# Performance work log

Measured on AMD Instinct MI355X. Metric: run time of the kernel, lower is better.

Reference implementation:

```python
import jax, jax.numpy as jnp
import numpy as np
from jax import lax

B, N1, F1 = 8, 8192, 64
N2, K = 1024, 32
RADIUS = 0.2
MLP_SIZES = [64, 64, 128]
IN_DIM = 3 + F1  # concat(local xyz, features)


def _glorot_uniform(key, fan_in, fan_out):
    lim = np.sqrt(6.0 / (fan_in + fan_out)).astype(np.float32)
    return jax.random.uniform(key, (fan_in, fan_out), jnp.float32, -lim, lim)


def setup_inputs() -> dict:
    key = jax.random.key(0)
    ks = jax.random.split(key, 2 + len(MLP_SIZES))
    xyz = jax.random.uniform(ks[0], (B, N1, 3), jnp.float32)
    features = jax.random.normal(ks[1], (B, N1, F1), jnp.float32)
    inp = {"xyz": xyz, "features": features}
    d = IN_DIM
    for i, m in enumerate(MLP_SIZES):
        inp[f"W{i}"] = _glorot_uniform(ks[2 + i], d, m)
        inp[f"b{i}"] = jnp.zeros((m,), jnp.float32)
        d = m
    return inp


def farthest_point_sample(xyz, n_sample):
    # xyz: (B, N, 3) -> (B, n_sample) int32 indices. Sequential greedy FPS via scan.
    Bb, N, _ = xyz.shape
    first = jnp.zeros((Bb,), jnp.int32)
    big = jnp.finfo(xyz.dtype).max

    def step(carry, _):
        min_d, last = carry
        p = jnp.take_along_axis(xyz, last[:, None, None], axis=1)  # (B,1,3)
        d = jnp.sum((xyz - p) ** 2, axis=-1)                        # (B,N)
        min_d = jnp.minimum(min_d, d)
        nxt = jnp.argmax(min_d, axis=1).astype(jnp.int32)
        return (min_d, nxt), nxt

    init = (jnp.full((Bb, N), big, xyz.dtype), first)
    _, rest = lax.scan(step, init, None, length=n_sample - 1)  # (n_sample-1, B)
    return jnp.concatenate([first[None, :], rest], axis=0).T    # (B, n_sample)


def knn_search(query, points, k, radius):
    # query: (B,N2,3), points: (B,N1,3) -> (B,N2,k) indices, radius-clamped
    q2 = jnp.sum(query ** 2, -1)[:, :, None]          # (B,N2,1)
    p2 = jnp.sum(points ** 2, -1)[:, None, :]         # (B,1,N1)
    qp = jnp.einsum('bqd,bnd->bqn', query, points)    # (B,N2,N1)
    d2 = q2 + p2 - 2.0 * qp
    neg, idx = lax.top_k(-d2, k)                       # k nearest
    d2k = -neg
    # neighbors beyond the radius are replaced by the closest neighbor (ball query)
    idx = jnp.where(d2k > radius * radius, idx[..., :1], idx)
    return idx, d2k


def _gather_pts(x, idx):
    # x: (B,N1,C), idx: (B,N2[,K]) -> batched gather along axis 1
    return jnp.take_along_axis(x, idx.reshape(x.shape[0], -1, 1), axis=1).reshape(
        idx.shape + (x.shape[-1],))


def reference(xyz, features, W0, b0, W1, b1, W2, b2):
    sel_idx = farthest_point_sample(xyz, N2)                    # (B,N2)
    selected_xyz = _gather_pts(xyz, sel_idx)                    # (B,N2,3)
    nbr_idx, _ = knn_search(selected_xyz, xyz, K, RADIUS)       # (B,N2,K)
    nbr_xyz = _gather_pts(xyz, nbr_idx) - selected_xyz[:, :, None, :]
    nbr_feat = _gather_pts(features, nbr_idx)                   # (B,N2,K,F1)
    h = jnp.concatenate([nbr_xyz, nbr_feat], axis=-1)           # (B,N2,K,3+F1)
    for W, b in ((W0, b0), (W1, b1), (W2, b2)):
        h = jax.nn.leaky_relu(jnp.einsum('bqkc,cm->bqkm', h, W) + b, 0.2)
    selected_features = jnp.max(h, axis=2)                      # (B,N2,F2)
    return selected_xyz, selected_features
```

## Files before the change

kernel.cpp:

```cpp
#include <hip/hip_runtime.h>

#define B_   8
#define N1_  8192
#define N2_  1024
#define K_   32
#define F1_  64
#define CIN_ 67
#define M1_  64
#define M2_  64
#define M3_  128
#define HSTR 40
#define FLTMAX 3.402823466e+38f

#define FNW  4
#define PPT  32

__device__ __forceinline__ unsigned f2key(float f) {
  unsigned u = __float_as_uint(f);
  return u ^ ((unsigned)((int)u >> 31) | 0x80000000u);
}

__device__ __forceinline__ unsigned dpp_umax_bcast(unsigned v) {
  unsigned o;
  o = (unsigned)__builtin_amdgcn_update_dpp(0, (int)v, 0x111, 0xf, 0xf, false); v = v > o ? v : o;
  o = (unsigned)__builtin_amdgcn_update_dpp(0, (int)v, 0x112, 0xf, 0xf, false); v = v > o ? v : o;
  o = (unsigned)__builtin_amdgcn_update_dpp(0, (int)v, 0x114, 0xf, 0xf, false); v = v > o ? v : o;
  o = (unsigned)__builtin_amdgcn_update_dpp(0, (int)v, 0x118, 0xf, 0xf, false); v = v > o ? v : o;
  o = (unsigned)__builtin_amdgcn_update_dpp(0, (int)v, 0x142, 0xf, 0xf, false); v = v > o ? v : o;
  o = (unsigned)__builtin_amdgcn_update_dpp(0, (int)v, 0x143, 0xf, 0xf, false); v = v > o ? v : o;
  return (unsigned)__builtin_amdgcn_readlane((int)v, 63);
}
__device__ __forceinline__ unsigned dpp_umin_bcast(unsigned v) {
  unsigned o;
  o = (unsigned)__builtin_amdgcn_update_dpp(-1, (int)v, 0x111, 0xf, 0xf, false); v = v < o ? v : o;
  o = (unsigned)__builtin_amdgcn_update_dpp(-1, (int)v, 0x112, 0xf, 0xf, false); v = v < o ? v : o;
  o = (unsigned)__builtin_amdgcn_update_dpp(-1, (int)v, 0x114, 0xf, 0xf, false); v = v < o ? v : o;
  o = (unsigned)__builtin_amdgcn_update_dpp(-1, (int)v, 0x118, 0xf, 0xf, false); v = v < o ? v : o;
  o = (unsigned)__builtin_amdgcn_update_dpp(-1, (int)v, 0x142, 0xf, 0xf, false); v = v < o ? v : o;
  o = (unsigned)__builtin_amdgcn_update_dpp(-1, (int)v, 0x143, 0xf, 0xf, false); v = v < o ? v : o;
  return (unsigned)__builtin_amdgcn_readlane((int)v, 63);
}

#define HS_ENC(f) (__float_as_uint(f) ^ 0xC0000000u)
#define HS_DEC(u) __uint_as_float((u) ^ 0xC0000000u)

__global__ __launch_bounds__(256, 1) void fused_kernel(
    const float* __restrict__ xyz, const float* __restrict__ feat,
    const float* __restrict__ w0g, const float* __restrict__ b0g,
    const float* __restrict__ w1g, const float* __restrict__ b1g,
    const float* __restrict__ w2g, const float* __restrict__ b2g,
    float* __restrict__ out_xyz, float* __restrict__ out_feat)
{
  __shared__ float4 wslot[2][FNW];
  __shared__ __align__(16) float buf0[CIN_*HSTR];
  __shared__ __align__(16) float buf1[M1_*HSTR];
  __shared__ float sval[2][4];
  __shared__ int   sidx[2][4];
  __shared__ float qsh[3];

  const int t = threadIdx.x;
  const int lane = t & 63;

  if (blockIdx.x < B_) {
    __builtin_amdgcn_s_setprio(3);
    const int b = blockIdx.x;
    const float* gxyz = xyz + (size_t)b * (N1_ * 3);
    float* oxyz = out_xyz + (size_t)b * (N2_ * 3);

    float x[PPT], y[PPT], z[PPT], md[PPT];
    {
      const float4* gs = (const float4*)gxyz;
#pragma unroll
      for (int w = 0; w < 24; ++w) {
        const float4 v = gs[t * 24 + w];
#pragma unroll
        for (int c = 0; c < 4; ++c) {
          const int p = w * 4 + c;
          const float val = (c == 0) ? v.x : (c == 1) ? v.y : (c == 2) ? v.z : v.w;
          const int j = p / 3, cc = p % 3;
          if (cc == 0) x[j] = val; else if (cc == 1) y[j] = val; else z[j] = val;
        }
      }
    }
#pragma unroll
    for (int j = 0; j < PPT; ++j) md[j] = FLTMAX;

    const int wv_ = t >> 6;
    if (lane == 0) { float4 s; s.x = -1.0f; s.y = 0.f; s.z = 0.f; s.w = 0.f; wslot[1][wv_] = s; }
    if (t == 0)   { float4 s; s.x = 1.0f; s.y = x[0]; s.z = y[0]; s.w = z[0]; wslot[1][0] = s; }
    __syncthreads();

    for (int i = 1; i < N2_; ++i) {
      const int p = i & 1;
      float4 wb = wslot[p][0];
#pragma unroll
      for (int u = 1; u < FNW; ++u) { const float4 s = wslot[p][u]; if (s.x > wb.x) wb = s; }
      const float px = wb.y, py = wb.z, pz = wb.w;
      if (t == 0) {
        const int g = (b << 10) + (i - 1);
        const int o = (i - 1) * 3;
        oxyz[o] = px; oxyz[o+1] = py; oxyz[o+2] = pz;
        unsigned* hs = (unsigned*)(out_feat + (size_t)g * M3_);
        atomicExch(&hs[0], HS_ENC(px));
        atomicExch(&hs[1], HS_ENC(py));
        atomicExch(&hs[2], HS_ENC(pz));
      }

      float bestv, bx, by, bz;
#pragma unroll
      for (int j = 0; j < PPT; ++j) {
        const float dx = __fsub_rn(x[j], px);
        const float dy = __fsub_rn(y[j], py);
        const float dz = __fsub_rn(z[j], pz);
        const float d  = __fadd_rn(__fadd_rn(__fmul_rn(dx,dx), __fmul_rn(dy,dy)), __fmul_rn(dz,dz));
        md[j] = fminf(md[j], d);
        if (j == 0) { bestv = md[0]; bx = x[0]; by = y[0]; bz = z[0]; }
        else {
          const bool c = md[j] > bestv;
          bestv = c ? md[j] : bestv;
          bx = c ? x[j] : bx; by = c ? y[j] : by; bz = c ? z[j] : bz;
        }
      }
      const unsigned key = f2key(bestv);
      const unsigned kmax = dpp_umax_bcast(key);
      const int fl = __ffsll(__ballot(key == kmax)) - 1;
      if (lane == fl) {
        float4 s; s.x = bestv; s.y = bx; s.z = by; s.w = bz;
        wslot[1 - p][wv_] = s;
      }
      __syncthreads();
    }
    if (t == 0) {
      float4 wb = wslot[0][0];
#pragma unroll
      for (int u = 1; u < FNW; ++u) { const float4 s = wslot[0][u]; if (s.x > wb.x) wb = s; }
      const int g = (b << 10) + (N2_ - 1);
      const int o = (N2_ - 1) * 3;
      oxyz[o] = wb.y; oxyz[o+1] = wb.z; oxyz[o+2] = wb.w;
      unsigned* hs = (unsigned*)(out_feat + (size_t)g * M3_);
      atomicExch(&hs[0], HS_ENC(wb.y));
      atomicExch(&hs[1], HS_ENC(wb.z));
      atomicExch(&hs[2], HS_ENC(wb.w));
    }
    return;
  }

  const int bq = blockIdx.x - B_;
  const int b  = bq >> 10;
  const float* gxyz = xyz + (size_t)b * (N1_ * 3);

  if (t == 0) {
    unsigned* hs = (unsigned*)(out_feat + (size_t)bq * M3_);
#pragma unroll
    for (int w = 0; w < 3; ++w) {
      unsigned v;
      do { __builtin_amdgcn_s_sleep(2); v = atomicOr(&hs[w], 0u); }
      while (v == 0u || v == 0xAAAAAAAAu);
      qsh[w] = HS_DEC(v);
    }
  }
  __syncthreads();
  const float qx = qsh[0], qy = qsh[1], qz = qsh[2];
  const float q2 = __fadd_rn(__fadd_rn(__fmul_rn(qx,qx), __fmul_rn(qy,qy)), __fmul_rn(qz,qz));

  float d2v[32];
  float m1 = FLTMAX, m2 = FLTMAX; int i1 = t*32, i2 = t*32;
  {
    const float4* gs = (const float4*)gxyz;
#pragma unroll
    for (int g8 = 0; g8 < 4; ++g8) {
      float f[24];
#pragma unroll
      for (int w = 0; w < 6; ++w) {
        const float4 v = gs[t * 24 + g8 * 6 + w];
        f[w*4+0] = v.x; f[w*4+1] = v.y; f[w*4+2] = v.z; f[w*4+3] = v.w;
      }
#pragma unroll
      for (int m = 0; m < 8; ++m) {
        const int j = g8 * 8 + m;
        const float px = f[3*m], py = f[3*m+1], pz = f[3*m+2];
        const float p2 = __fadd_rn(__fadd_rn(__fmul_rn(px,px), __fmul_rn(py,py)), __fmul_rn(pz,pz));
        const float qp = __fadd_rn(__fadd_rn(__fmul_rn(qx,px), __fmul_rn(qy,py)), __fmul_rn(qz,pz));
        const float d  = __fsub_rn(__fadd_rn(q2, p2), __fmul_rn(2.0f, qp));
        d2v[j] = d;
        const int idx = t*32 + j;
        const bool c1 = d < m1;
        const bool c2 = d < m2;
        const float nm2 = c1 ? m1 : (c2 ? d : m2);
        const int   ni2 = c1 ? i1 : (c2 ? idx : i2);
        m1 = c1 ? d : m1; i1 = c1 ? idx : i1;
        m2 = nm2; i2 = ni2;
      }
    }
  }

  int myk_idx = 0; float myk_d = 0.0f; int k0_idx = 0;
  unsigned removed = 0u; bool have2 = true;
  for (int kk = 0; kk < K_; ++kk) {
    const int p = kk & 1;
    const unsigned key = f2key(m1);
    const unsigned kmin = dpp_umin_bcast(key);
    const int fl = __ffsll(__ballot(key == kmin)) - 1;
    if (lane == fl) { sval[p][t >> 6] = m1; sidx[p][t >> 6] = i1; }
    __syncthreads();
    float wv = sval[p][0]; int wi = sidx[p][0];
#pragma unroll
    for (int u = 1; u < 4; ++u) {
      const float v = sval[p][u]; const int ii = sidx[p][u];
      if (v < wv || (v == wv && ii < wi)) { wv = v; wi = ii; }
    }
    wi &= (N1_ - 1);
    if ((t >> 3) == kk) { myk_idx = wi; myk_d = wv; }
    if (kk == 0) k0_idx = wi;
    if (kk < K_ - 1 && t == (wi >> 5)) {
      removed |= 1u << (wi & 31);
      if (have2) { m1 = m2; i1 = i2; have2 = false; }
      else {
        m1 = FLTMAX; i1 = t*32; m2 = FLTMAX; i2 = t*32;
#pragma unroll
        for (int j = 0; j < 32; ++j) {
          const float d = ((removed >> j) & 1u) ? FLTMAX : d2v[j];
          const int idx = t*32 + j;
          const bool c1 = d < m1;
          const bool c2 = d < m2;
          const float nm2 = c1 ? m1 : (c2 ? d : m2);
          const int   ni2 = c1 ? i1 : (c2 ? idx : i2);
          m1 = c1 ? d : m1; i1 = c1 ? idx : i1;
          m2 = nm2; i2 = ni2;
        }
        have2 = true;
      }
    }
  }

  {
    const int k = t >> 3, fg = t & 7;
    int nk = myk_idx;
    if (myk_d > 0.04f) nk = k0_idx;
    nk &= (N1_ - 1);
    const float* frow = feat + ((size_t)(b * N1_ + nk)) * F1_ + fg * 8;
    const float4 f0 = *(const float4*)frow;
    const float4 f1 = *(const float4*)(frow + 4);
    const int fb = 3 + fg * 8;
    buf0[(fb+0)*HSTR + k] = f0.x;
    buf0[(fb+1)*HSTR + k] = f0.y;
    buf0[(fb+2)*HSTR + k] = f0.z;
    buf0[(fb+3)*HSTR + k] = f0.w;
    buf0[(fb+4)*HSTR + k] = f1.x;
    buf0[(fb+5)*HSTR + k] = f1.y;
    buf0[(fb+6)*HSTR + k] = f1.z;
    buf0[(fb+7)*HSTR + k] = f1.w;
    if (fg < 3) {
      const float pc = gxyz[(size_t)nk * 3 + fg];
      const float qc = (fg == 0) ? qx : (fg == 1) ? qy : qz;
      buf0[fg * HSTR + k] = __fsub_rn(pc, qc);
    }
  }
  __syncthreads();

#define LEAKY_STORE2(acc, mi_, biasg, hout) { \
    const float bb = biasg[mg*2 + (mi_)]; \
    float4 v; \
    v.x = acc.x + bb; v.x = fmaxf(v.x, 0.2f*v.x); \
    v.y = acc.y + bb; v.y = fmaxf(v.y, 0.2f*v.y); \
    v.z = acc.z + bb; v.z = fmaxf(v.z, 0.2f*v.z); \
    v.w = acc.w + bb; v.w = fmaxf(v.w, 0.2f*v.w); \
    *(float4*)&hout[(mg*2 + (mi_)) * HSTR + kq * 4] = v; }

  {
    const int kq = t & 7, mg = t >> 3;
    float4 a0 = {0,0,0,0}, a1 = {0,0,0,0};
#pragma unroll 4
    for (int c = 0; c < CIN_; ++c) {
      const float2 wp = *(const float2*)&w0g[c * M1_ + mg * 2];
      const float4 h  = *(const float4*)&buf0[c * HSTR + kq * 4];
      a0.x += h.x*wp.x; a0.y += h.y*wp.x; a0.z += h.z*wp.x; a0.w += h.w*wp.x;
      a1.x += h.x*wp.y; a1.y += h.y*wp.y; a1.z += h.z*wp.y; a1.w += h.w*wp.y;
    }
    LEAKY_STORE2(a0, 0, b0g, buf1) LEAKY_STORE2(a1, 1, b0g, buf1)
  }
  __syncthreads();

  {
    const int kq = t & 7, mg = t >> 3;
    float4 a0 = {0,0,0,0}, a1 = {0,0,0,0};
#pragma unroll 4
    for (int c = 0; c < M1_; ++c) {
      const float2 wp = *(const float2*)&w1g[c * M2_ + mg * 2];
      const float4 h  = *(const float4*)&buf1[c * HSTR + kq * 4];
      a0.x += h.x*wp.x; a0.y += h.y*wp.x; a0.z += h.z*wp.x; a0.w += h.w*wp.x;
      a1.x += h.x*wp.y; a1.y += h.y*wp.y; a1.z += h.z*wp.y; a1.w += h.w*wp.y;
    }
    LEAKY_STORE2(a0, 0, b1g, buf0) LEAKY_STORE2(a1, 1, b1g, buf0)
  }
#undef LEAKY_STORE2
  __syncthreads();

  {
    const int kq = t & 7, mg = t >> 3;
    float4 a0 = {0,0,0,0}, a1 = {0,0,0,0}, a2 = {0,0,0,0}, a3 = {0,0,0,0};
#pragma unroll 4
    for (int c = 0; c < M2_; ++c) {
      const float4 wp = *(const float4*)&w2g[c * M3_ + mg * 4];
      const float4 h  = *(const float4*)&buf0[c * HSTR + kq * 4];
      a0.x += h.x*wp.x; a0.y += h.y*wp.x; a0.z += h.z*wp.x; a0.w += h.w*wp.x;
      a1.x += h.x*wp.y; a1.y += h.y*wp.y; a1.z += h.z*wp.y; a1.w += h.w*wp.y;
      a2.x += h.x*wp.z; a2.y += h.y*wp.z; a2.z += h.z*wp.z; a2.w += h.w*wp.z;
      a3.x += h.x*wp.w; a3.y += h.y*wp.w; a3.z += h.z*wp.w; a3.w += h.w*wp.w;
    }
    float vm[4];
#define BIAS_LEAKY_HMAX(acc, mi_) { \
      const float bb = b2g[mg*4 + (mi_)]; \
      float vx = acc.x + bb; vx = fmaxf(vx, 0.2f*vx); \
      float vy = acc.y + bb; vy = fmaxf(vy, 0.2f*vy); \
      float vz = acc.z + bb; vz = fmaxf(vz, 0.2f*vz); \
      float vw = acc.w + bb; vw = fmaxf(vw, 0.2f*vw); \
      vm[mi_] = fmaxf(fmaxf(vx, vy), fmaxf(vz, vw)); }
    BIAS_LEAKY_HMAX(a0, 0) BIAS_LEAKY_HMAX(a1, 1) BIAS_LEAKY_HMAX(a2, 2) BIAS_LEAKY_HMAX(a3, 3)
#undef BIAS_LEAKY_HMAX
#pragma unroll
    for (int m = 1; m <= 4; m <<= 1) {
      vm[0] = fmaxf(vm[0], __shfl_xor(vm[0], m, 64));
      vm[1] = fmaxf(vm[1], __shfl_xor(vm[1], m, 64));
      vm[2] = fmaxf(vm[2], __shfl_xor(vm[2], m, 64));
      vm[3] = fmaxf(vm[3], __shfl_xor(vm[3], m, 64));
    }
    if (kq == 0) {
      float4 o; o.x = vm[0]; o.y = vm[1]; o.z = vm[2]; o.w = vm[3];
      *(float4*)&out_feat[(size_t)bq * M3_ + mg * 4] = o;
    }
  }
}

extern "C" void kernel_launch(void* const* d_in, const int* in_sizes, int n_in,
                              void* d_out, int out_size, void* d_ws, size_t ws_size,
                              hipStream_t stream) {
  const float* xyz  = (const float*)d_in[0];
  const float* feat = (const float*)d_in[1];
  const float* w0   = (const float*)d_in[2];
  const float* b0   = (const float*)d_in[3];
  const float* w1   = (const float*)d_in[4];
  const float* b1   = (const float*)d_in[5];
  const float* w2   = (const float*)d_in[6];
  const float* b2   = (const float*)d_in[7];

  float* out_xyz  = (float*)d_out;
  float* out_feat = out_xyz + B_ * N2_ * 3;

  fused_kernel<<<B_ + B_ * N2_, 256, 0, stream>>>(xyz, feat, w0, b0, w1, b1, w2, b2,
                                                  out_xyz, out_feat);
}
```

Measured before the change: 1.474 ms.

## Double threads per block to 512 and re-split FPS, kNN and MLP work

Raises the block size from 256 to 512 threads. Each thread now handles 16 points instead of 32 in FPS and kNN, and the kNN selection, feature gather and the three MLP layers are re-partitioned so each thread computes half as many output channels. The intent is to cut the per-thread serial latency of the sequential FPS loop and of the per-query top-k passes. In exchange, every reduction step spans twice as many waves and barriers, and the FPS blocks, which spin-wait against the query blocks, may see occupancy change.

```diff
diff --git a/kernel.cpp b/kernel.cpp
--- a/kernel.cpp
+++ b/kernel.cpp
@@ -12,8 +12,10 @@
 #define HSTR 40
 #define FLTMAX 3.402823466e+38f
 
-#define FNW  4
-#define PPT  32
+#define TPB  512
+#define FNW  (TPB/64)
+#define PPT  (N1_/TPB)
+#define PPC  16
 
 __device__ __forceinline__ unsigned f2key(float f) {
   unsigned u = __float_as_uint(f);
@@ -44,7 +46,7 @@
 #define HS_ENC(f) (__float_as_uint(f) ^ 0xC0000000u)
 #define HS_DEC(u) __uint_as_float((u) ^ 0xC0000000u)
 
-__global__ __launch_bounds__(256, 1) void fused_kernel(
+__global__ __launch_bounds__(TPB, 1) void fused_kernel(
     const float* __restrict__ xyz, const float* __restrict__ feat,
     const float* __restrict__ w0g, const float* __restrict__ b0g,
     const float* __restrict__ w1g, const float* __restrict__ b1g,
@@ -54,12 +56,13 @@
   __shared__ float4 wslot[2][FNW];
   __shared__ __align__(16) float buf0[CIN_*HSTR];
   __shared__ __align__(16) float buf1[M1_*HSTR];
-  __shared__ float sval[2][4];
-  __shared__ int   sidx[2][4];
+  __shared__ float sval[2][FNW];
+  __shared__ int   sidx[2][FNW];
   __shared__ float qsh[3];
 
   const int t = threadIdx.x;
   const int lane = t & 63;
+  const int wv_ = t >> 6;
 
   if (blockIdx.x < B_) {
     __builtin_amdgcn_s_setprio(3);
@@ -71,8 +74,8 @@
     {
       const float4* gs = (const float4*)gxyz;
 #pragma unroll
-      for (int w = 0; w < 24; ++w) {
-        const float4 v = gs[t * 24 + w];
+      for (int w = 0; w < 12; ++w) {
+        const float4 v = gs[t * 12 + w];
 #pragma unroll
         for (int c = 0; c < 4; ++c) {
           const int p = w * 4 + c;
@@ -85,7 +88,6 @@
 #pragma unroll
     for (int j = 0; j < PPT; ++j) md[j] = FLTMAX;
 
-    const int wv_ = t >> 6;
     if (lane == 0) { float4 s; s.x = -1.0f; s.y = 0.f; s.z = 0.f; s.w = 0.f; wslot[1][wv_] = s; }
     if (t == 0)   { float4 s; s.x = 1.0f; s.y = x[0]; s.z = y[0]; s.w = z[0]; wslot[1][0] = s; }
     __syncthreads();
@@ -163,16 +165,16 @@
   const float qx = qsh[0], qy = qsh[1], qz = qsh[2];
   const float q2 = __fadd_rn(__fadd_rn(__fmul_rn(qx,qx), __fmul_rn(qy,qy)), __fmul_rn(qz,qz));
 
-  float d2v[32];
-  float m1 = FLTMAX, m2 = FLTMAX; int i1 = t*32, i2 = t*32;
+  float d2v[PPC];
+  float m1 = FLTMAX, m2 = FLTMAX; int i1 = t*PPC, i2 = t*PPC;
   {
     const float4* gs = (const float4*)gxyz;
 #pragma unroll
-    for (int g8 = 0; g8 < 4; ++g8) {
+    for (int g8 = 0; g8 < 2; ++g8) {
       float f[24];
 #pragma unroll
       for (int w = 0; w < 6; ++w) {
-        const float4 v = gs[t * 24 + g8 * 6 + w];
+        const float4 v = gs[t * 12 + g8 * 6 + w];
         f[w*4+0] = v.x; f[w*4+1] = v.y; f[w*4+2] = v.z; f[w*4+3] = v.w;
       }
 #pragma unroll
@@ -183,7 +185,7 @@
         const float qp = __fadd_rn(__fadd_rn(__fmul_rn(qx,px), __fmul_rn(qy,py)), __fmul_rn(qz,pz));
         const float d  = __fsub_rn(__fadd_rn(q2, p2), __fmul_rn(2.0f, qp));
         d2v[j] = d;
-        const int idx = t*32 + j;
+        const int idx = t*PPC + j;
         const bool c1 = d < m1;
         const bool c2 = d < m2;
         const float nm2 = c1 ? m1 : (c2 ? d : m2);
@@ -201,26 +203,26 @@
     const unsigned key = f2key(m1);
     const unsigned kmin = dpp_umin_bcast(key);
     const int fl = __ffsll(__ballot(key == kmin)) - 1;
-    if (lane == fl) { sval[p][t >> 6] = m1; sidx[p][t >> 6] = i1; }
+    if (lane == fl) { sval[p][wv_] = m1; sidx[p][wv_] = i1; }
     __syncthreads();
     float wv = sval[p][0]; int wi = sidx[p][0];
 #pragma unroll
-    for (int u = 1; u < 4; ++u) {
+    for (int u = 1; u < FNW; ++u) {
       const float v = sval[p][u]; const int ii = sidx[p][u];
       if (v < wv || (v == wv && ii < wi)) { wv = v; wi = ii; }
     }
     wi &= (N1_ - 1);
-    if ((t >> 3) == kk) { myk_idx = wi; myk_d = wv; }
+    if ((t >> 4) == kk) { myk_idx = wi; myk_d = wv; }
     if (kk == 0) k0_idx = wi;
-    if (kk < K_ - 1 && t == (wi >> 5)) {
-      removed |= 1u << (wi & 31);
+    if (kk < K_ - 1 && t == (wi >> 4)) {
+      removed |= 1u << (wi & 15);
       if (have2) { m1 = m2; i1 = i2; have2 = false; }
       else {
-        m1 = FLTMAX; i1 = t*32; m2 = FLTMAX; i2 = t*32;
-#pragma unroll
-        for (int j = 0; j < 32; ++j) {
+        m1 = FLTMAX; i1 = t*PPC; m2 = FLTMAX; i2 = t*PPC;
+#pragma unroll
+        for (int j = 0; j < PPC; ++j) {
           const float d = ((removed >> j) & 1u) ? FLTMAX : d2v[j];
-          const int idx = t*32 + j;
+          const int idx = t*PPC + j;
           const bool c1 = d < m1;
           const bool c2 = d < m2;
           const float nm2 = c1 ? m1 : (c2 ? d : m2);
@@ -234,22 +236,16 @@
   }
 
   {
-    const int k = t >> 3, fg = t & 7;
+    const int k = t >> 4, fg = t & 15;
     int nk = myk_idx;
     if (myk_d > 0.04f) nk = k0_idx;
     nk &= (N1_ - 1);
-    const float* frow = feat + ((size_t)(b * N1_ + nk)) * F1_ + fg * 8;
-    const float4 f0 = *(const float4*)frow;
-    const float4 f1 = *(const float4*)(frow + 4);
-    const int fb = 3 + fg * 8;
+    const float4 f0 = *(const float4*)(feat + ((size_t)(b * N1_ + nk)) * F1_ + fg * 4);
+    const int fb = 3 + fg * 4;
     buf0[(fb+0)*HSTR + k] = f0.x;
     buf0[(fb+1)*HSTR + k] = f0.y;
     buf0[(fb+2)*HSTR + k] = f0.z;
     buf0[(fb+3)*HSTR + k] = f0.w;
-    buf0[(fb+4)*HSTR + k] = f1.x;
-    buf0[(fb+5)*HSTR + k] = f1.y;
-    buf0[(fb+6)*HSTR + k] = f1.z;
-    buf0[(fb+7)*HSTR + k] = f1.w;
     if (fg < 3) {
       const float pc = gxyz[(size_t)nk * 3 + fg];
       const float qc = (fg == 0) ? qx : (fg == 1) ? qy : qz;
@@ -258,76 +254,70 @@
   }
   __syncthreads();
 
-#define LEAKY_STORE2(acc, mi_, biasg, hout) { \
-    const float bb = biasg[mg*2 + (mi_)]; \
+#define LEAKY_STORE1(acc, biasg, hout) { \
+    const float bb = biasg[mg]; \
     float4 v; \
     v.x = acc.x + bb; v.x = fmaxf(v.x, 0.2f*v.x); \
     v.y = acc.y + bb; v.y = fmaxf(v.y, 0.2f*v.y); \
     v.z = acc.z + bb; v.z = fmaxf(v.z, 0.2f*v.z); \
     v.w = acc.w + bb; v.w = fmaxf(v.w, 0.2f*v.w); \
-    *(float4*)&hout[(mg*2 + (mi_)) * HSTR + kq * 4] = v; }
+    *(float4*)&hout[mg * HSTR + kq * 4] = v; }
+
+  {
+    const int kq = t & 7, mg = t >> 3;
+    float4 a0 = {0,0,0,0};
+#pragma unroll 4
+    for (int c = 0; c < CIN_; ++c) {
+      const float w = w0g[c * M1_ + mg];
+      const float4 h = *(const float4*)&buf0[c * HSTR + kq * 4];
+      a0.x += h.x*w; a0.y += h.y*w; a0.z += h.z*w; a0.w += h.w*w;
+    }
+    LEAKY_STORE1(a0, b0g, buf1)
+  }
+  __syncthreads();
+
+  {
+    const int kq = t & 7, mg = t >> 3;
+    float4 a0 = {0,0,0,0};
+#pragma unroll 4
+    for (int c = 0; c < M1_; ++c) {
+      const float w = w1g[c * M2_ + mg];
+      const float4 h = *(const float4*)&buf1[c * HSTR + kq * 4];
+      a0.x += h.x*w; a0.y += h.y*w; a0.z += h.z*w; a0.w += h.w*w;
+    }
+    LEAKY_STORE1(a0, b1g, buf0)
+  }
+#undef LEAKY_STORE1
+  __syncthreads();
 
   {
     const int kq = t & 7, mg = t >> 3;
     float4 a0 = {0,0,0,0}, a1 = {0,0,0,0};
 #pragma unroll 4
-    for (int c = 0; c < CIN_; ++c) {
-      const float2 wp = *(const float2*)&w0g[c * M1_ + mg * 2];
+    for (int c = 0; c < M2_; ++c) {
+      const float2 wp = *(const float2*)&w2g[c * M3_ + mg * 2];
       const float4 h  = *(const float4*)&buf0[c * HSTR + kq * 4];
       a0.x += h.x*wp.x; a0.y += h.y*wp.x; a0.z += h.z*wp.x; a0.w += h.w*wp.x;
       a1.x += h.x*wp.y; a1.y += h.y*wp.y; a1.z += h.z*wp.y; a1.w += h.w*wp.y;
     }
-    LEAKY_STORE2(a0, 0, b0g, buf1) LEAKY_STORE2(a1, 1, b0g, buf1)
-  }
-  __syncthreads();
-
-  {
-    const int kq = t & 7, mg = t >> 3;
-    float4 a0 = {0,0,0,0}, a1 = {0,0,0,0};
-#pragma unroll 4
-    for (int c = 0; c < M1_; ++c) {
-      const float2 wp = *(const float2*)&w1g[c * M2_ + mg * 2];
-      const float4 h  = *(const float4*)&buf1[c * HSTR + kq * 4];
-      a0.x += h.x*wp.x; a0.y += h.y*wp.x; a0.z += h.z*wp.x; a0.w += h.w*wp.x;
-      a1.x += h.x*wp.y; a1.y += h.y*wp.y; a1.z += h.z*wp.y; a1.w += h.w*wp.y;
-    }
-    LEAKY_STORE2(a0, 0, b1g, buf0) LEAKY_STORE2(a1, 1, b1g, buf0)
-  }
-#undef LEAKY_STORE2
-  __syncthreads();
-
-  {
-    const int kq = t & 7, mg = t >> 3;
-    float4 a0 = {0,0,0,0}, a1 = {0,0,0,0}, a2 = {0,0,0,0}, a3 = {0,0,0,0};
-#pragma unroll 4
-    for (int c = 0; c < M2_; ++c) {
-      const float4 wp = *(const float4*)&w2g[c * M3_ + mg * 4];
-      const float4 h  = *(const float4*)&buf0[c * HSTR + kq * 4];
-      a0.x += h.x*wp.x; a0.y += h.y*wp.x; a0.z += h.z*wp.x; a0.w += h.w*wp.x;
-      a1.x += h.x*wp.y; a1.y += h.y*wp.y; a1.z += h.z*wp.y; a1.w += h.w*wp.y;
-      a2.x += h.x*wp.z; a2.y += h.y*wp.z; a2.z += h.z*wp.z; a2.w += h.w*wp.z;
-      a3.x += h.x*wp.w; a3.y += h.y*wp.w; a3.z += h.z*wp.w; a3.w += h.w*wp.w;
-    }
-    float vm[4];
+    float vm[2];
 #define BIAS_LEAKY_HMAX(acc, mi_) { \
-      const float bb = b2g[mg*4 + (mi_)]; \
+      const float bb = b2g[mg*2 + (mi_)]; \
       float vx = acc.x + bb; vx = fmaxf(vx, 0.2f*vx); \
       float vy = acc.y + bb; vy = fmaxf(vy, 0.2f*vy); \
       float vz = acc.z + bb; vz = fmaxf(vz, 0.2f*vz); \
       float vw = acc.w + bb; vw = fmaxf(vw, 0.2f*vw); \
       vm[mi_] = fmaxf(fmaxf(vx, vy), fmaxf(vz, vw)); }
-    BIAS_LEAKY_HMAX(a0, 0) BIAS_LEAKY_HMAX(a1, 1) BIAS_LEAKY_HMAX(a2, 2) BIAS_LEAKY_HMAX(a3, 3)
+    BIAS_LEAKY_HMAX(a0, 0) BIAS_LEAKY_HMAX(a1, 1)
 #undef BIAS_LEAKY_HMAX
 #pragma unroll
     for (int m = 1; m <= 4; m <<= 1) {
       vm[0] = fmaxf(vm[0], __shfl_xor(vm[0], m, 64));
       vm[1] = fmaxf(vm[1], __shfl_xor(vm[1], m, 64));
-      vm[2] = fmaxf(vm[2], __shfl_xor(vm[2], m, 64));
-      vm[3] = fmaxf(vm[3], __shfl_xor(vm[3], m, 64));
     }
     if (kq == 0) {
-      float4 o; o.x = vm[0]; o.y = vm[1]; o.z = vm[2]; o.w = vm[3];
-      *(float4*)&out_feat[(size_t)bq * M3_ + mg * 4] = o;
+      float2 o; o.x = vm[0]; o.y = vm[1];
+      *(float2*)&out_feat[(size_t)bq * M3_ + mg * 2] = o;
     }
   }
 }
@@ -347,6 +337,6 @@
   float* out_xyz  = (float*)d_out;
   float* out_feat = out_xyz + B_ * N2_ * 3;
 
-  fused_kernel<<<B_ + B_ * N2_, 256, 0, stream>>>(xyz, feat, w0, b0, w1, b1, w2, b2,
+  fused_kernel<<<B_ + B_ * N2_, TPB, 0, stream>>>(xyz, feat, w0, b0, w1, b1, w2, b2,
                                                   out_xyz, out_feat);
 }
```

New measurement: 1.706 ms. +15.7%, slower.

## Split farthest point sampling across four cooperating blocks per batch

Applied to the files above, without the earlier changes.

Each batch's FPS now runs on four blocks, each holding a quarter of the points. The blocks exchange their per-iteration winners through global memory slots tagged with the iteration number, and each block picks the global argmax. This cuts per-thread distance work but adds a cross-block global atomic handshake on every iteration. It relies on all FPS blocks being co-resident, and on the slots in the workspace not holding stale matching tags.

```diff
diff --git a/kernel.cpp b/kernel.cpp
--- a/kernel.cpp
+++ b/kernel.cpp
@@ -12,12 +12,15 @@
 #define HSTR 40
 #define FLTMAX 3.402823466e+38f
 
-#define FNW  4
-#define PPT  32
+#define PB_  (B_*4)
+#define PPTP 8
 
 __device__ __forceinline__ unsigned f2key(float f) {
   unsigned u = __float_as_uint(f);
   return u ^ ((unsigned)((int)u >> 31) | 0x80000000u);
+}
+__device__ __forceinline__ float readlane_f(float v, int l) {
+  return __int_as_float(__builtin_amdgcn_readlane(__float_as_int(v), l));
 }
 
 __device__ __forceinline__ unsigned dpp_umax_bcast(unsigned v) {
@@ -49,9 +52,11 @@
     const float* __restrict__ w0g, const float* __restrict__ b0g,
     const float* __restrict__ w1g, const float* __restrict__ b1g,
     const float* __restrict__ w2g, const float* __restrict__ b2g,
-    float* __restrict__ out_xyz, float* __restrict__ out_feat)
+    float* __restrict__ out_xyz, float* __restrict__ out_feat,
+    unsigned long long* __restrict__ slots)
 {
-  __shared__ float4 wslot[2][FNW];
+  __shared__ float4 wslot[4];
+  __shared__ float4 gwin;
   __shared__ __align__(16) float buf0[CIN_*HSTR];
   __shared__ __align__(16) float buf1[M1_*HSTR];
   __shared__ float sval[2][4];
@@ -60,19 +65,20 @@
 
   const int t = threadIdx.x;
   const int lane = t & 63;
-
-  if (blockIdx.x < B_) {
+  const int wv_ = t >> 6;
+
+  if (blockIdx.x < PB_) {
     __builtin_amdgcn_s_setprio(3);
-    const int b = blockIdx.x;
+    const int b = blockIdx.x >> 2, s = blockIdx.x & 3;
     const float* gxyz = xyz + (size_t)b * (N1_ * 3);
     float* oxyz = out_xyz + (size_t)b * (N2_ * 3);
 
-    float x[PPT], y[PPT], z[PPT], md[PPT];
+    float x[PPTP], y[PPTP], z[PPTP], md[PPTP];
     {
       const float4* gs = (const float4*)gxyz;
 #pragma unroll
-      for (int w = 0; w < 24; ++w) {
-        const float4 v = gs[t * 24 + w];
+      for (int w = 0; w < 6; ++w) {
+        const float4 v = gs[s * 1536 + t * 6 + w];
 #pragma unroll
         for (int c = 0; c < 4; ++c) {
           const int p = w * 4 + c;
@@ -83,32 +89,24 @@
       }
     }
 #pragma unroll
-    for (int j = 0; j < PPT; ++j) md[j] = FLTMAX;
-
-    const int wv_ = t >> 6;
-    if (lane == 0) { float4 s; s.x = -1.0f; s.y = 0.f; s.z = 0.f; s.w = 0.f; wslot[1][wv_] = s; }
-    if (t == 0)   { float4 s; s.x = 1.0f; s.y = x[0]; s.z = y[0]; s.w = z[0]; wslot[1][0] = s; }
-    __syncthreads();
-
-    for (int i = 1; i < N2_; ++i) {
-      const int p = i & 1;
-      float4 wb = wslot[p][0];
-#pragma unroll
-      for (int u = 1; u < FNW; ++u) { const float4 s = wslot[p][u]; if (s.x > wb.x) wb = s; }
-      const float px = wb.y, py = wb.z, pz = wb.w;
-      if (t == 0) {
-        const int g = (b << 10) + (i - 1);
-        const int o = (i - 1) * 3;
+    for (int j = 0; j < PPTP; ++j) md[j] = FLTMAX;
+
+    float px = gxyz[0], py = gxyz[1], pz = gxyz[2];
+
+    for (int i = 0;; ++i) {
+      if (s == 0 && t == 0) {
+        const int o = i * 3;
         oxyz[o] = px; oxyz[o+1] = py; oxyz[o+2] = pz;
-        unsigned* hs = (unsigned*)(out_feat + (size_t)g * M3_);
+        unsigned* hs = (unsigned*)(out_feat + (size_t)((b << 10) + i) * M3_);
         atomicExch(&hs[0], HS_ENC(px));
         atomicExch(&hs[1], HS_ENC(py));
         atomicExch(&hs[2], HS_ENC(pz));
       }
+      if (i == N2_ - 1) break;
 
       float bestv, bx, by, bz;
 #pragma unroll
-      for (int j = 0; j < PPT; ++j) {
+      for (int j = 0; j < PPTP; ++j) {
         const float dx = __fsub_rn(x[j], px);
         const float dy = __fsub_rn(y[j], py);
         const float dz = __fsub_rn(z[j], pz);
@@ -121,31 +119,58 @@
           bx = c ? x[j] : bx; by = c ? y[j] : by; bz = c ? z[j] : bz;
         }
       }
-      const unsigned key = f2key(bestv);
-      const unsigned kmax = dpp_umax_bcast(key);
-      const int fl = __ffsll(__ballot(key == kmax)) - 1;
-      if (lane == fl) {
-        float4 s; s.x = bestv; s.y = bx; s.z = by; s.w = bz;
-        wslot[1 - p][wv_] = s;
+      {
+        const unsigned key = f2key(bestv);
+        const unsigned kmax = dpp_umax_bcast(key);
+        const int fl = __ffsll(__ballot(key == kmax)) - 1;
+        if (lane == fl) {
+          float4 sl; sl.x = bestv; sl.y = bx; sl.z = by; sl.w = bz;
+          wslot[wv_] = sl;
+        }
       }
       __syncthreads();
-    }
-    if (t == 0) {
-      float4 wb = wslot[0][0];
-#pragma unroll
-      for (int u = 1; u < FNW; ++u) { const float4 s = wslot[0][u]; if (s.x > wb.x) wb = s; }
-      const int g = (b << 10) + (N2_ - 1);
-      const int o = (N2_ - 1) * 3;
-      oxyz[o] = wb.y; oxyz[o+1] = wb.z; oxyz[o+2] = wb.w;
-      unsigned* hs = (unsigned*)(out_feat + (size_t)g * M3_);
-      atomicExch(&hs[0], HS_ENC(wb.y));
-      atomicExch(&hs[1], HS_ENC(wb.z));
-      atomicExch(&hs[2], HS_ENC(wb.w));
+
+      if (wv_ == 0) {
+        float4 wb = wslot[0];
+#pragma unroll
+        for (int u = 1; u < 4; ++u) { const float4 sl = wslot[u]; if (sl.x > wb.x) wb = sl; }
+        const unsigned long long st = ((unsigned long long)(unsigned)(i + 1)) << 32;
+        if (t == 0) {
+          unsigned long long* sl = slots + (((b * 2 + ((i + 1) & 1)) * 4 + s) << 2);
+          atomicExch(&sl[0], st | __float_as_uint(wb.x));
+          atomicExch(&sl[1], st | __float_as_uint(wb.y));
+          atomicExch(&sl[2], st | __float_as_uint(wb.z));
+          atomicExch(&sl[3], st | __float_as_uint(wb.w));
+        }
+        float fv, fx, fy, fz;
+        if (t < 4) {
+          unsigned long long* sl = slots + (((b * 2 + ((i + 1) & 1)) * 4 + t) << 2);
+          const unsigned sw = (unsigned)(i + 1);
+          unsigned long long q;
+          do { q = atomicOr(&sl[0], 0ull); } while ((unsigned)(q >> 32) != sw);
+          fv = __uint_as_float((unsigned)q);
+          do { q = atomicOr(&sl[1], 0ull); } while ((unsigned)(q >> 32) != sw);
+          fx = __uint_as_float((unsigned)q);
+          do { q = atomicOr(&sl[2], 0ull); } while ((unsigned)(q >> 32) != sw);
+          fy = __uint_as_float((unsigned)q);
+          do { q = atomicOr(&sl[3], 0ull); } while ((unsigned)(q >> 32) != sw);
+          fz = __uint_as_float((unsigned)q);
+        }
+        float bv = readlane_f(fv, 0), cx = readlane_f(fx, 0), cy = readlane_f(fy, 0), cz = readlane_f(fz, 0);
+#pragma unroll
+        for (int u = 1; u < 4; ++u) {
+          const float vv = readlane_f(fv, u);
+          if (vv > bv) { bv = vv; cx = readlane_f(fx, u); cy = readlane_f(fy, u); cz = readlane_f(fz, u); }
+        }
+        if (t == 0) { float4 g; g.x = cx; g.y = cy; g.z = cz; g.w = bv; gwin = g; }
+      }
+      __syncthreads();
+      px = gwin.x; py = gwin.y; pz = gwin.z;
     }
     return;
   }
 
-  const int bq = blockIdx.x - B_;
+  const int bq = blockIdx.x - PB_;
   const int b  = bq >> 10;
   const float* gxyz = xyz + (size_t)b * (N1_ * 3);
 
@@ -346,7 +371,8 @@
 
   float* out_xyz  = (float*)d_out;
   float* out_feat = out_xyz + B_ * N2_ * 3;
-
-  fused_kernel<<<B_ + B_ * N2_, 256, 0, stream>>>(xyz, feat, w0, b0, w1, b1, w2, b2,
-                                                  out_xyz, out_feat);
-}
+  unsigned long long* slots = (unsigned long long*)d_ws;
+
+  fused_kernel<<<PB_ + B_ * N2_, 256, 0, stream>>>(xyz, feat, w0, b0, w1, b1, w2, b2,
+                                                   out_xyz, out_feat, slots);
+}
```

Result: slower. 2.040 ms (+38.4%).

## Replace per-iteration block barrier in FPS with LDS stamp-based wave handoff

Applied to the files above, without the earlier changes.

The farthest point sampling loop used a __syncthreads per iteration to exchange per-wave argmax candidates through a double-buffered shared slot array. This version has each wave publish its candidate plus an iteration stamp into LDS (aliasing buf0) and spin on the four stamps. Lanes read the candidates in parallel, and readlane picks the global winner. This removes the full block barrier from the 1023-step serial critical path, at the cost of busy-wait polling and reliance on volatile LDS ordering between data and stamp writes.

```diff
diff --git a/kernel.cpp b/kernel.cpp
--- a/kernel.cpp
+++ b/kernel.cpp
@@ -12,12 +12,14 @@
 #define HSTR 40
 #define FLTMAX 3.402823466e+38f
 
-#define FNW  4
 #define PPT  32
 
 __device__ __forceinline__ unsigned f2key(float f) {
   unsigned u = __float_as_uint(f);
   return u ^ ((unsigned)((int)u >> 31) | 0x80000000u);
+}
+__device__ __forceinline__ float readlane_f(float v, int l) {
+  return __int_as_float(__builtin_amdgcn_readlane(__float_as_int(v), l));
 }
 
 __device__ __forceinline__ unsigned dpp_umax_bcast(unsigned v) {
@@ -51,7 +53,6 @@
     const float* __restrict__ w2g, const float* __restrict__ b2g,
     float* __restrict__ out_xyz, float* __restrict__ out_feat)
 {
-  __shared__ float4 wslot[2][FNW];
   __shared__ __align__(16) float buf0[CIN_*HSTR];
   __shared__ __align__(16) float buf1[M1_*HSTR];
   __shared__ float sval[2][4];
@@ -60,12 +61,18 @@
 
   const int t = threadIdx.x;
   const int lane = t & 63;
+  const int wv_ = t >> 6;
 
   if (blockIdx.x < B_) {
     __builtin_amdgcn_s_setprio(3);
     const int b = blockIdx.x;
     const float* gxyz = xyz + (size_t)b * (N1_ * 3);
     float* oxyz = out_xyz + (size_t)b * (N2_ * 3);
+
+    float4* pslot = (float4*)buf0;
+    volatile int* pstamp = (volatile int*)(buf0 + 32);
+
+    if (t < 8) pstamp[t] = 0;
 
     float x[PPT], y[PPT], z[PPT], md[PPT];
     {
@@ -84,28 +91,18 @@
     }
 #pragma unroll
     for (int j = 0; j < PPT; ++j) md[j] = FLTMAX;
-
-    const int wv_ = t >> 6;
-    if (lane == 0) { float4 s; s.x = -1.0f; s.y = 0.f; s.z = 0.f; s.w = 0.f; wslot[1][wv_] = s; }
-    if (t == 0)   { float4 s; s.x = 1.0f; s.y = x[0]; s.z = y[0]; s.w = z[0]; wslot[1][0] = s; }
     __syncthreads();
 
+    float px = gxyz[0], py = gxyz[1], pz = gxyz[2];
+    if (t == 0) {
+      oxyz[0] = px; oxyz[1] = py; oxyz[2] = pz;
+      unsigned* hs = (unsigned*)(out_feat + (size_t)(b << 10) * M3_);
+      atomicExch(&hs[0], HS_ENC(px));
+      atomicExch(&hs[1], HS_ENC(py));
+      atomicExch(&hs[2], HS_ENC(pz));
+    }
+
     for (int i = 1; i < N2_; ++i) {
-      const int p = i & 1;
-      float4 wb = wslot[p][0];
-#pragma unroll
-      for (int u = 1; u < FNW; ++u) { const float4 s = wslot[p][u]; if (s.x > wb.x) wb = s; }
-      const float px = wb.y, py = wb.z, pz = wb.w;
-      if (t == 0) {
-        const int g = (b << 10) + (i - 1);
-        const int o = (i - 1) * 3;
-        oxyz[o] = px; oxyz[o+1] = py; oxyz[o+2] = pz;
-        unsigned* hs = (unsigned*)(out_feat + (size_t)g * M3_);
-        atomicExch(&hs[0], HS_ENC(px));
-        atomicExch(&hs[1], HS_ENC(py));
-        atomicExch(&hs[2], HS_ENC(pz));
-      }
-
       float bestv, bx, by, bz;
 #pragma unroll
       for (int j = 0; j < PPT; ++j) {
@@ -124,23 +121,31 @@
       const unsigned key = f2key(bestv);
       const unsigned kmax = dpp_umax_bcast(key);
       const int fl = __ffsll(__ballot(key == kmax)) - 1;
+      const int par = (i & 1) * 4;
       if (lane == fl) {
-        float4 s; s.x = bestv; s.y = bx; s.z = by; s.w = bz;
-        wslot[1 - p][wv_] = s;
-      }
-      __syncthreads();
-    }
-    if (t == 0) {
-      float4 wb = wslot[0][0];
-#pragma unroll
-      for (int u = 1; u < FNW; ++u) { const float4 s = wslot[0][u]; if (s.x > wb.x) wb = s; }
-      const int g = (b << 10) + (N2_ - 1);
-      const int o = (N2_ - 1) * 3;
-      oxyz[o] = wb.y; oxyz[o+1] = wb.z; oxyz[o+2] = wb.w;
-      unsigned* hs = (unsigned*)(out_feat + (size_t)g * M3_);
-      atomicExch(&hs[0], HS_ENC(wb.y));
-      atomicExch(&hs[1], HS_ENC(wb.z));
-      atomicExch(&hs[2], HS_ENC(wb.w));
+        float4 pl; pl.x = bestv; pl.y = bx; pl.z = by; pl.w = bz;
+        pslot[par + wv_] = pl;
+        pstamp[par + wv_] = i;
+      }
+      const int sb = par + (lane & 3);
+      while (pstamp[sb] != i) { }
+      volatile float* pf = (volatile float*)&pslot[sb];
+      const float vv = pf[0], vx = pf[1], vy = pf[2], vz = pf[3];
+      const float c0 = readlane_f(vv, 0), c1 = readlane_f(vv, 1);
+      const float c2 = readlane_f(vv, 2), c3 = readlane_f(vv, 3);
+      int ws = 0; float bv = c0;
+      if (c1 > bv) { bv = c1; ws = 1; }
+      if (c2 > bv) { bv = c2; ws = 2; }
+      if (c3 > bv) { bv = c3; ws = 3; }
+      px = readlane_f(vx, ws); py = readlane_f(vy, ws); pz = readlane_f(vz, ws);
+      if (t == 0) {
+        const int o = i * 3;
+        oxyz[o] = px; oxyz[o+1] = py; oxyz[o+2] = pz;
+        unsigned* hs = (unsigned*)(out_feat + (size_t)((b << 10) + i) * M3_);
+        atomicExch(&hs[0], HS_ENC(px));
+        atomicExch(&hs[1], HS_ENC(py));
+        atomicExch(&hs[2], HS_ENC(pz));
+      }
     }
     return;
   }
```

Measured after the change: 1.531 ms. 3.9% more time.
